# Kernel optimization log

Hardware: AMD Instinct MI355X
Metric: run time of the kernel (lower is better)

## Reference

```python
import jax, jax.numpy as jnp
import numpy as np

EPS = 1e-5

def bn(x, gamma, beta, axes):
    # Training-mode batch norm: normalize over batch(+spatial) axes, channel-last layout.
    m = x.mean(axes, keepdims=True)
    v = x.var(axes, keepdims=True)
    return gamma * (x - m) * jax.lax.rsqrt(v + EPS) + beta

def spa_group(k, xyz, feat):
    # PCT-style grouping: k-NN in xyz space, concat(neighbor-center, center).
    # xyz: (B,N,3)  feat: (B,N,C)  ->  (B,N,k,2C)
    sq = jnp.sum(xyz * xyz, axis=-1)  # (B,N)
    d = sq[:, :, None] + sq[:, None, :] - 2.0 * jnp.einsum('bnd,bmd->bnm', xyz, xyz)
    _, idx = jax.lax.top_k(-d, k)  # (B,N,k) nearest-neighbor indices (includes self)
    grouped = jax.vmap(lambda f, i: f[i])(feat, idx)  # (B,N,k,C) irregular gather
    center = feat[:, :, None, :]
    return jnp.concatenate([grouped - center, jnp.broadcast_to(center, grouped.shape)], axis=-1)

def local_op(x, w1, g1, b1, w2, g2, b2):
    # x: (B,N,K,Ci) -> conv1x1/BN/ReLU x2 over the K window, then max-pool over K -> (B,N,Co)
    h = jnp.einsum('bnkc,oc->bnko', x, w1)
    h = jax.nn.relu(bn(h, g1, b1, (0, 1, 2)))
    h = jnp.einsum('bnkc,oc->bnko', h, w2)
    h = jax.nn.relu(bn(h, g2, b2, (0, 1, 2)))
    return h.max(axis=2)

def setup_inputs():
    key = jax.random.key(0)
    ks = jax.random.split(key, 7)
    B, N = 4, 2048
    d_i, d_h1, d_h2, d_h3, d_o = 3, 64, 256, 512, 1024
    def w(k_, o, i):
        return jax.random.normal(k_, (o, i), jnp.float32) * (1.0 / np.sqrt(i))
    return {
        'xyz': jax.random.normal(ks[0], (B, N, d_i), jnp.float32),
        'w_c1': w(ks[1], d_h1, d_i), 'g_c1': jnp.ones((d_h1,), jnp.float32), 'b_c1': jnp.zeros((d_h1,), jnp.float32),
        'w_c2': w(ks[2], d_h2, d_h1), 'g_c2': jnp.ones((d_h2,), jnp.float32), 'b_c2': jnp.zeros((d_h2,), jnp.float32),
        'w_l0a': w(ks[3], d_h3, d_h3), 'g_l0a': jnp.ones((d_h3,), jnp.float32), 'b_l0a': jnp.zeros((d_h3,), jnp.float32),
        'w_l0b': w(ks[4], d_h3, d_h3), 'g_l0b': jnp.ones((d_h3,), jnp.float32), 'b_l0b': jnp.zeros((d_h3,), jnp.float32),
        'w_l1a': w(ks[5], d_o, d_o), 'g_l1a': jnp.ones((d_o,), jnp.float32), 'b_l1a': jnp.zeros((d_o,), jnp.float32),
        'w_l1b': w(ks[6], d_o, d_o), 'g_l1b': jnp.ones((d_o,), jnp.float32), 'b_l1b': jnp.zeros((d_o,), jnp.float32),
        'k': 8,
    }

def reference(xyz, w_c1, g_c1, b_c1, w_c2, g_c2, b_c2,
              w_l0a, g_l0a, b_l0a, w_l0b, g_l0b, b_l0b,
              w_l1a, g_l1a, b_l1a, w_l1b, g_l1b, b_l1b, k):
    # Stem: conv1x1-BN-ReLU x2 in (B,N,C) layout (equivalent to torch (B,C,N) with BN over (0,2))
    h = jax.nn.relu(bn(jnp.einsum('bnc,oc->bno', xyz, w_c1), g_c1, b_c1, (0, 1)))
    h = jax.nn.relu(bn(jnp.einsum('bnc,oc->bno', h, w_c2), g_c2, b_c2, (0, 1)))
    g = spa_group(k, xyz, h)                                   # (B,N,k,512)
    h = local_op(g, w_l0a, g_l0a, b_l0a, w_l0b, g_l0b, b_l0b)  # (B,N,512)
    g = spa_group(k, xyz, h)                                   # (B,N,k,1024)
    h = local_op(g, w_l1a, g_l1a, b_l1a, w_l1b, g_l1b, b_l1b)  # (B,N,1024)
    return jnp.transpose(h, (0, 2, 1))  # (B, d_o, N) to match torch output layout
```

## Files before the change

### kernel.cpp

```cpp
#include <hip/hip_runtime.h>

typedef unsigned short u16;
typedef __attribute__((ext_vector_type(8))) short s16x8;
typedef __attribute__((ext_vector_type(8))) __bf16 bf16x8;
typedef __attribute__((ext_vector_type(8))) unsigned short u16x8;
typedef __attribute__((ext_vector_type(4))) float f32x4;

#define BN_EPS 1e-5f

__device__ u16   g_Z[(size_t)65536 * 1024];
__device__ float g_pooled[(size_t)8192 * 1024];
__device__ float g_h2pre[8192 * 256];
__device__ u16   g_h2b[8192 * 256];
__device__ u16   g_hl0b[8192 * 512];
__device__ float g_y1[8192 * 64];
__device__ u16   g_wm0a[512 * 512];
__device__ u16   g_w0b[512 * 512];
__device__ u16   g_wm1a[1024 * 1024];
__device__ u16   g_w1b[1024 * 1024];
__device__ int   g_nidx[65536];
__device__ float g_st[24 * 1024];

#define S(i) (g_st + (i) * 1024)

static __device__ __forceinline__ float bf2f(u16 u) {
  unsigned int x = ((unsigned int)u) << 16;
  return __builtin_bit_cast(float, x);
}
static __device__ __forceinline__ u16 f2bf(float f) {
  unsigned int x = __builtin_bit_cast(unsigned int, f);
  x += 0x7fffu + ((x >> 16) & 1u);
  return (u16)(x >> 16);
}
static __device__ __forceinline__ f32x4 mfma16x16(s16x8 a, s16x8 b, f32x4 c) {
  return __builtin_amdgcn_mfma_f32_16x16x32_bf16(
      __builtin_bit_cast(bf16x8, a), __builtin_bit_cast(bf16x8, b), c, 0, 0, 0);
}
static __device__ __forceinline__ void gl_lds16(const void* g, void* l) {
  __builtin_amdgcn_global_load_lds((const __attribute__((address_space(1))) void*)g,
                                   (__attribute__((address_space(3))) void*)l, 16, 0, 0);
}

__global__ void k_zero() {
  int i = blockIdx.x * 256 + threadIdx.x;
  if (i < 12 * 1024) g_st[i] = 0.f;
}

__global__ void k_lin1(const float* __restrict__ xyz, const float* __restrict__ w) {
  __shared__ float ls[64], lq[64];
  int t = threadIdx.x;
  if (t < 64) { ls[t] = 0.f; lq[t] = 0.f; }
  __syncthreads();
  int e = blockIdx.x * 256 + t;
  int row = e >> 6, ch = e & 63;
  float x0 = xyz[row * 3], x1 = xyz[row * 3 + 1], x2 = xyz[row * 3 + 2];
  float v = x0 * w[ch * 3] + x1 * w[ch * 3 + 1] + x2 * w[ch * 3 + 2];
  g_y1[e] = v;
  atomicAdd(&ls[ch], v);
  atomicAdd(&lq[ch], v * v);
  __syncthreads();
  if (t < 64) { atomicAdd(&S(0)[t], ls[t]); atomicAdd(&S(1)[t], lq[t]); }
}

__global__ void k_stats(const float* __restrict__ g, const float* __restrict__ b,
                        int si_s, int si_q, int si_sc, int si_bi, float invcnt) {
  int c = blockIdx.x * 64 + threadIdx.x;
  float m = S(si_s)[c] * invcnt;
  float v = S(si_q)[c] * invcnt - m * m;
  float sc = g[c] * rsqrtf(v + BN_EPS);
  S(si_sc)[c] = sc;
  S(si_bi)[c] = b[c] - m * sc;
}

__global__ void k_lin2(const float* __restrict__ w) {
  __shared__ float hrow[64];
  int t = threadIdx.x;
  float wr[64];
#pragma unroll
  for (int i = 0; i < 64; i++) wr[i] = w[t * 64 + i];
  const float* sc1 = S(12);
  const float* bi1 = S(13);
  float ps = 0.f, pq = 0.f;
  int r0 = blockIdx.x * 16;
  for (int r = 0; r < 16; r++) {
    if (t < 64) {
      float v = g_y1[(r0 + r) * 64 + t];
      v = v * sc1[t] + bi1[t];
      hrow[t] = v > 0.f ? v : 0.f;
    }
    __syncthreads();
    float acc = 0.f;
#pragma unroll
    for (int i = 0; i < 64; i++) acc += hrow[i] * wr[i];
    g_h2pre[(r0 + r) * 256 + t] = acc;
    ps += acc;
    pq += acc * acc;
    __syncthreads();
  }
  atomicAdd(&S(2)[t], ps);
  atomicAdd(&S(3)[t], pq);
}

__global__ void k_bnrelu_h2() {
  int i = blockIdx.x * 256 + threadIdx.x;
  if (i >= 8192 * 256) return;
  int c = i & 255;
  float v = g_h2pre[i] * S(14)[c] + S(15)[c];
  g_h2b[i] = f2bf(v > 0.f ? v : 0.f);
}

__global__ __launch_bounds__(256) void k_knn(const float* __restrict__ xyz) {
  int t = threadIdx.x, lane = t & 63, w = t >> 6;
  int qn = blockIdx.x * 4 + w;
  int b = qn >> 11;
  const float* xb = xyz + (size_t)b * 2048 * 3;
  int ql = qn & 2047;
  float qx = xb[ql * 3], qy = xb[ql * 3 + 1], qz = xb[ql * 3 + 2];
  float qsq = qx * qx + qy * qy + qz * qz;

  float bd[8];
  int bi[8];
#pragma unroll
  for (int i = 0; i < 8; i++) { bd[i] = 1e30f; bi[i] = 0x7fffffff; }

#pragma unroll 4
  for (int i = 0; i < 32; i++) {
    int j = lane + i * 64;
    float x = xb[j * 3], y = xb[j * 3 + 1], z = xb[j * 3 + 2];
    float sq = x * x + y * y + z * z;
    float d = qsq + sq - 2.0f * (qx * x + qy * y + qz * z);
    if (d < bd[7]) {
      bd[7] = d; bi[7] = j;
#pragma unroll
      for (int p = 7; p > 0; p--) {
        if (bd[p] < bd[p - 1]) {
          float td = bd[p]; bd[p] = bd[p - 1]; bd[p - 1] = td;
          int ti = bi[p]; bi[p] = bi[p - 1]; bi[p - 1] = ti;
        }
      }
    }
  }

  int keep = 0;
#pragma unroll
  for (int r = 0; r < 8; r++) {
    float md = bd[0];
    int mi = bi[0];
#pragma unroll
    for (int s = 1; s < 64; s <<= 1) {
      float od = __shfl_xor(md, s, 64);
      int oi = __shfl_xor(mi, s, 64);
      if (od < md || (od == md && oi < mi)) { md = od; mi = oi; }
    }
    bool own = (bd[0] == md) && (bi[0] == mi);
    if (own) {
#pragma unroll
      for (int p = 0; p < 7; p++) { bd[p] = bd[p + 1]; bi[p] = bi[p + 1]; }
      bd[7] = 1e30f; bi[7] = 0x7fffffff;
    }
    if (lane == r) keep = mi;
  }
  if (lane < 8) g_nidx[qn * 8 + lane] = b * 2048 + keep;
}

__global__ void k_prep_w(const float* __restrict__ src, int which, int K, int half, int n) {
  int i = blockIdx.x * 256 + threadIdx.x;
  if (i >= n) return;
  int col = i % K;
  float v = src[i];
  if (half && col >= half) v -= src[i - half];
  u16* dst = which == 0 ? g_wm0a : which == 1 ? g_w0b : which == 2 ? g_wm1a : g_w1b;
  dst[i] = f2bf(v);
}


#define GEMM_PRO()                                                     \
  int t = threadIdx.x, lane = t & 63, w = t >> 6;                      \
  int chunk = gridDim.x >> 3;                                          \
  int idx = ((int)blockIdx.x & 7) * chunk + ((int)blockIdx.x >> 3);    \
  int bx = idx & ((1 << lbx) - 1), by = idx >> lbx;                    \
  int wm = w >> 2, wn = w & 3;                                         \
  int l15 = lane & 15, lq = lane >> 4;                                 \
  int gcs = (((lane & 3) ^ ((lane >> 3) & 3))) * 8;                    \
  int rA0 = w * 16 + (lane >> 2), rA1 = rA0 + 128;                     \
  int ldsA0 = w * 512, ldsA1 = 4096 + w * 512;                         \
  int ksw = (lq ^ ((l15 >> 1) & 3)) * 8;                               \
  f32x4 acc[8][4];                                                     \
  _Pragma("unroll") for (int m = 0; m < 8; m++)                        \
  _Pragma("unroll") for (int n = 0; n < 4; n++)                        \
      acc[m][n] = f32x4{0.f, 0.f, 0.f, 0.f};

#define GEMM_LOOP(STG)                                                   \
  STG(0, 0) STG(1, 1) STG(2, 2)                                          \
  asm volatile("s_waitcnt vmcnt(8)" ::: "memory");                       \
  __builtin_amdgcn_s_barrier();                                          \
  asm volatile("" ::: "memory");                                         \
  for (int ks = 0; ks < nk; ks++) {                                      \
    int b = ks & 3;                                                      \
    int kst = (ks + 3 < nk) ? ks + 3 : nk - 1;                           \
    STG(kst, (ks + 3) & 3)                                               \
    s16x8 af[8], bf[4];                                                  \
    _Pragma("unroll") for (int m = 0; m < 8; m++)                        \
        af[m] = *(const s16x8*)&As[b][(wm * 128 + m * 16 + l15) * 32 + ksw]; \
    _Pragma("unroll") for (int n = 0; n < 4; n++)                        \
        bf[n] = *(const s16x8*)&Bs[b][(wn * 64 + n * 16 + l15) * 32 + ksw];  \
    __builtin_amdgcn_s_setprio(1);                                       \
    _Pragma("unroll") for (int m = 0; m < 8; m++)                        \
    _Pragma("unroll") for (int n = 0; n < 4; n++)                        \
        acc[m][n] = mfma16x16(af[m], bf[n], acc[m][n]);                  \
    __builtin_amdgcn_s_setprio(0);                                       \
    asm volatile("s_waitcnt vmcnt(8)" ::: "memory");                     \
    __builtin_amdgcn_s_barrier();                                        \
    asm volatile("" ::: "memory");                                       \
  }

#define GEMM_STATS(si_s, si_q)                                           \
  if (t < 256) { cs[t] = 0.f; cq[t] = 0.f; }                             \
  __syncthreads();                                                       \
  _Pragma("unroll") for (int n = 0; n < 4; n++) {                        \
    float ssum = 0.f, ssq = 0.f;                                         \
    _Pragma("unroll") for (int m = 0; m < 8; m++)                        \
    _Pragma("unroll") for (int j = 0; j < 4; j++) {                      \
      float v = acc[m][n][j];                                            \
      ssum += v;                                                         \
      ssq += v * v;                                                      \
    }                                                                    \
    int col = wn * 64 + n * 16 + l15;                                    \
    atomicAdd(&cs[col], ssum);                                           \
    atomicAdd(&cq[col], ssq);                                            \
  }                                                                      \
  __syncthreads();                                                       \
  if (t < 256) {                                                         \
    atomicAdd(&S(si_s)[bx * 256 + t], cs[t]);                            \
    atomicAdd(&S(si_q)[bx * 256 + t], cq[t]);                            \
  }

__global__ __launch_bounds__(512) void k_gg8(int layer, int C, int N, int si_s,
                                             int si_q, int lbx) {
  __shared__ u16 As[4][8192];
  __shared__ u16 Bs[4][8192];
  __shared__ float cs[256], cq[256];
  const u16* feat = layer == 0 ? g_h2b : g_hl0b;
  const u16* W = layer == 0 ? g_wm0a : g_wm1a;
  GEMM_PRO();
  int K = 2 * C, nk = K >> 5;
  int RA0 = by * 256 + rA0, RA1 = RA0 + 128;
  int nb0 = g_nidx[RA0], nb1 = g_nidx[RA1];
  int ct0 = RA0 >> 3, ct1 = RA1 >> 3;
  const u16* srB0 = W + (size_t)(bx * 256 + rA0) * K + gcs;
  const u16* srB1 = W + (size_t)(bx * 256 + rA1) * K + gcs;

#define STG_G(KT, BUF)                                                        \
  {                                                                           \
    int kg_ = (KT) * 32;                                                      \
    const u16 *sa0, *sa1;                                                     \
    if (kg_ < C) {                                                            \
      sa0 = feat + (size_t)nb0 * C + kg_ + gcs;                               \
      sa1 = feat + (size_t)nb1 * C + kg_ + gcs;                               \
    } else {                                                                  \
      sa0 = feat + (size_t)ct0 * C + (kg_ - C) + gcs;                         \
      sa1 = feat + (size_t)ct1 * C + (kg_ - C) + gcs;                         \
    }                                                                         \
    gl_lds16(sa0, &As[BUF][ldsA0]);                                           \
    gl_lds16(sa1, &As[BUF][ldsA1]);                                           \
    gl_lds16(srB0 + kg_, &Bs[BUF][ldsA0]);                                    \
    gl_lds16(srB1 + kg_, &Bs[BUF][ldsA1]);                                    \
  }

  GEMM_LOOP(STG_G)
#undef STG_G

#pragma unroll
  for (int m = 0; m < 8; m++) {
    int rbase = by * 256 + wm * 128 + m * 16 + lq * 4;
#pragma unroll
    for (int n = 0; n < 4; n++) {
      int col = bx * 256 + wn * 64 + n * 16 + l15;
#pragma unroll
      for (int j = 0; j < 4; j++)
        g_Z[(size_t)(rbase + j) * N + col] = f2bf(acc[m][n][j]);
    }
  }
  GEMM_STATS(si_s, si_q)
}

__global__ __launch_bounds__(512) void k_gp8(int layer, int K, int N, int si_s,
                                             int si_q, int lbx) {
  __shared__ u16 As[4][8192];
  __shared__ u16 Bs[4][8192];
  __shared__ float cs[256], cq[256];
  const u16* W = layer == 0 ? g_w0b : g_w1b;
  GEMM_PRO();
  int nk = K >> 5;
  const u16* srA0 = g_Z + (size_t)(by * 256 + rA0) * K + gcs;
  const u16* srA1 = g_Z + (size_t)(by * 256 + rA1) * K + gcs;
  const u16* srB0 = W + (size_t)(bx * 256 + rA0) * K + gcs;
  const u16* srB1 = W + (size_t)(bx * 256 + rA1) * K + gcs;

#define STG_P(KT, BUF)                                                        \
  {                                                                           \
    int kg_ = (KT) * 32;                                                      \
    gl_lds16(srA0 + kg_, &As[BUF][ldsA0]);                                    \
    gl_lds16(srA1 + kg_, &As[BUF][ldsA1]);                                    \
    gl_lds16(srB0 + kg_, &Bs[BUF][ldsA0]);                                    \
    gl_lds16(srB1 + kg_, &Bs[BUF][ldsA1]);                                    \
  }

  GEMM_LOOP(STG_P)
#undef STG_P

#pragma unroll
  for (int m = 0; m < 8; m++) {
    int prow = by * 32 + wm * 16 + m * 2 + (lq >> 1);
#pragma unroll
    for (int n = 0; n < 4; n++) {
      float v4 = fmaxf(fmaxf(acc[m][n][0], acc[m][n][1]), fmaxf(acc[m][n][2], acc[m][n][3]));
      float v8 = fmaxf(v4, __shfl_xor(v4, 16, 64));
      if ((lane & 16) == 0) {
        int col = bx * 256 + wn * 64 + n * 16 + l15;
        g_pooled[(size_t)prow * N + col] = v8;
      }
    }
  }
  GEMM_STATS(si_s, si_q)
}

__global__ void k_bnrelu_z(int si_sc, int si_bi, int cmask, size_t n8) {
  size_t i = (size_t)blockIdx.x * 256 + threadIdx.x;
  size_t stride = (size_t)gridDim.x * 256;
  const float* sc = S(si_sc);
  const float* bi = S(si_bi);
  for (; i < n8; i += stride) {
    u16x8 v = *(const u16x8*)(g_Z + i * 8);
    int c0 = (int)((i * 8) & (size_t)cmask);
    u16x8 o;
#pragma unroll
    for (int j = 0; j < 8; j++) {
      float f = bf2f(v[j]) * sc[c0 + j] + bi[c0 + j];
      o[j] = f2bf(f > 0.f ? f : 0.f);
    }
    *(u16x8*)(g_Z + i * 8) = o;
  }
}

__global__ void k_bnrelu_pool() {
  int i = blockIdx.x * 256 + threadIdx.x;
  if (i >= 8192 * 512) return;
  int c = i & 511;
  float v = g_pooled[i] * S(18)[c] + S(19)[c];
  g_hl0b[i] = f2bf(v > 0.f ? v : 0.f);
}

__global__ void k_final_t(float* __restrict__ out) {
  __shared__ float tile[64][65];
  int b = blockIdx.z;
  int nb = blockIdx.y;
  int cb = blockIdx.x;
  int t = threadIdx.x;
  int cl = t & 63;
  int c = cb * 64 + cl;
  float sc = S(22)[c], bi = S(23)[c];
  for (int nl = t >> 6; nl < 64; nl += 4) {
    float v = g_pooled[(size_t)(b * 2048 + nb * 64 + nl) * 1024 + c] * sc + bi;
    tile[nl][cl] = v > 0.f ? v : 0.f;
  }
  __syncthreads();
  int nl2 = t & 63;
  for (int ci = t >> 6; ci < 64; ci += 4) {
    out[((size_t)b * 1024 + cb * 64 + ci) * 2048 + nb * 64 + nl2] = tile[nl2][ci];
  }
}

extern "C" void kernel_launch(void* const* d_in, const int* in_sizes, int n_in,
                              void* d_out, int out_size, void* d_ws, size_t ws_size,
                              hipStream_t stream) {
  const float* xyz  = (const float*)d_in[0];
  const float* w_c1 = (const float*)d_in[1];
  const float* g_c1 = (const float*)d_in[2];
  const float* b_c1 = (const float*)d_in[3];
  const float* w_c2 = (const float*)d_in[4];
  const float* g_c2 = (const float*)d_in[5];
  const float* b_c2 = (const float*)d_in[6];
  const float* w_l0a = (const float*)d_in[7];
  const float* g_l0a = (const float*)d_in[8];
  const float* b_l0a = (const float*)d_in[9];
  const float* w_l0b = (const float*)d_in[10];
  const float* g_l0b = (const float*)d_in[11];
  const float* b_l0b = (const float*)d_in[12];
  const float* w_l1a = (const float*)d_in[13];
  const float* g_l1a = (const float*)d_in[14];
  const float* b_l1a = (const float*)d_in[15];
  const float* w_l1b = (const float*)d_in[16];
  const float* g_l1b = (const float*)d_in[17];
  const float* b_l1b = (const float*)d_in[18];
  float* out = (float*)d_out;

  k_zero<<<48, 256, 0, stream>>>();

  k_lin1<<<2048, 256, 0, stream>>>(xyz, w_c1);
  k_stats<<<1, 64, 0, stream>>>(g_c1, b_c1, 0, 1, 12, 13, 1.f / 8192.f);
  k_lin2<<<512, 256, 0, stream>>>(w_c2);
  k_stats<<<4, 64, 0, stream>>>(g_c2, b_c2, 2, 3, 14, 15, 1.f / 8192.f);
  k_bnrelu_h2<<<8192, 256, 0, stream>>>();

  k_knn<<<2048, 256, 0, stream>>>(xyz);

  k_prep_w<<<1024, 256, 0, stream>>>(w_l0a, 0, 512, 256, 262144);
  k_prep_w<<<1024, 256, 0, stream>>>(w_l0b, 1, 512, 0, 262144);
  k_prep_w<<<4096, 256, 0, stream>>>(w_l1a, 2, 1024, 512, 1048576);
  k_prep_w<<<4096, 256, 0, stream>>>(w_l1b, 3, 1024, 0, 1048576);

  k_gg8<<<512, 512, 0, stream>>>(0, 256, 512, 4, 5, 1);
  k_stats<<<8, 64, 0, stream>>>(g_l0a, b_l0a, 4, 5, 16, 17, 1.f / 65536.f);
  k_bnrelu_z<<<2048, 256, 0, stream>>>(16, 17, 511, (size_t)65536 * 512 / 8);
  k_gp8<<<512, 512, 0, stream>>>(0, 512, 512, 6, 7, 1);
  k_stats<<<8, 64, 0, stream>>>(g_l0b, b_l0b, 6, 7, 18, 19, 1.f / 65536.f);
  k_bnrelu_pool<<<16384, 256, 0, stream>>>();

  k_gg8<<<1024, 512, 0, stream>>>(1, 512, 1024, 8, 9, 2);
  k_stats<<<16, 64, 0, stream>>>(g_l1a, b_l1a, 8, 9, 20, 21, 1.f / 65536.f);
  k_bnrelu_z<<<2048, 256, 0, stream>>>(20, 21, 1023, (size_t)65536 * 1024 / 8);
  k_gp8<<<1024, 512, 0, stream>>>(1, 1024, 1024, 10, 11, 2);
  k_stats<<<16, 64, 0, stream>>>(g_l1b, b_l1b, 10, 11, 22, 23, 1.f / 65536.f);
  k_final_t<<<dim3(16, 32, 4), 256, 0, stream>>>(out);
}
```

Measured before the change: 897.6 us.

## Apply first local conv per point before gather, then combine gathered outputs

The first conv of each local_op is linear, so W·[f_nb - f_c, f_c] is split into W1·f_nb + (W2-W1)·f_c. Both products are now computed once per point (8192 rows) by a dense GEMM into a new buffer, replacing the per-neighbor GEMM over 65536 gathered rows with doubled K. A new combine kernel gathers the neighbor and center halves, adds them, writes Z in bf16 and accumulates the BN statistics. This cuts the matmul FLOPs for the first conv by roughly 8x, at the cost of an extra bf16 rounding of the intermediate sums and a memory-bound gather pass.

```diff
diff --git a/kernel.cpp b/kernel.cpp
--- a/kernel.cpp
+++ b/kernel.cpp
@@ -9,14 +9,15 @@
 #define BN_EPS 1e-5f
 
 __device__ u16   g_Z[(size_t)65536 * 1024];
+__device__ u16   g_F[(size_t)8192 * 2048];
 __device__ float g_pooled[(size_t)8192 * 1024];
 __device__ float g_h2pre[8192 * 256];
 __device__ u16   g_h2b[8192 * 256];
 __device__ u16   g_hl0b[8192 * 512];
 __device__ float g_y1[8192 * 64];
-__device__ u16   g_wm0a[512 * 512];
+__device__ u16   g_wm0a[1024 * 256];
 __device__ u16   g_w0b[512 * 512];
-__device__ u16   g_wm1a[1024 * 1024];
+__device__ u16   g_wm1a[2048 * 512];
 __device__ u16   g_w1b[1024 * 1024];
 __device__ int   g_nidx[65536];
 __device__ float g_st[24 * 1024];
@@ -163,13 +164,22 @@
   if (lane < 8) g_nidx[qn * 8 + lane] = b * 2048 + keep;
 }
 
-__global__ void k_prep_w(const float* __restrict__ src, int which, int K, int half, int n) {
+__global__ void k_prep_w(const float* __restrict__ src, int which, int n) {
   int i = blockIdx.x * 256 + threadIdx.x;
   if (i >= n) return;
-  int col = i % K;
-  float v = src[i];
-  if (half && col >= half) v -= src[i - half];
-  u16* dst = which == 0 ? g_wm0a : which == 1 ? g_w0b : which == 2 ? g_wm1a : g_w1b;
+  u16* dst = which == 1 ? g_w0b : g_w1b;
+  dst[i] = f2bf(src[i]);
+}
+
+__global__ void k_prep_wst(const float* __restrict__ src, int which, int lc, int N, int n) {
+  int i = blockIdx.x * 256 + threadIdx.x;
+  if (i >= n) return;
+  int C = 1 << lc;
+  int r = i >> lc, c = i & (C - 1);
+  float v;
+  if (r < N) v = src[r * 2 * C + c];
+  else { int o = r - N; v = src[o * 2 * C + C + c] - src[o * 2 * C + c]; }
+  u16* dst = which == 0 ? g_wm0a : g_wm1a;
   dst[i] = f2bf(v);
 }
 
@@ -235,40 +245,29 @@
     atomicAdd(&S(si_q)[bx * 256 + t], cq[t]);                            \
   }
 
-__global__ __launch_bounds__(512) void k_gg8(int layer, int C, int N, int si_s,
-                                             int si_q, int lbx) {
+__global__ __launch_bounds__(512) void k_fgemm(int layer, int C, int N2, int lbx) {
   __shared__ u16 As[4][8192];
   __shared__ u16 Bs[4][8192];
-  __shared__ float cs[256], cq[256];
   const u16* feat = layer == 0 ? g_h2b : g_hl0b;
   const u16* W = layer == 0 ? g_wm0a : g_wm1a;
   GEMM_PRO();
-  int K = 2 * C, nk = K >> 5;
-  int RA0 = by * 256 + rA0, RA1 = RA0 + 128;
-  int nb0 = g_nidx[RA0], nb1 = g_nidx[RA1];
-  int ct0 = RA0 >> 3, ct1 = RA1 >> 3;
-  const u16* srB0 = W + (size_t)(bx * 256 + rA0) * K + gcs;
-  const u16* srB1 = W + (size_t)(bx * 256 + rA1) * K + gcs;
-
-#define STG_G(KT, BUF)                                                        \
+  int nk = C >> 5;
+  const u16* srA0 = feat + (size_t)(by * 256 + rA0) * C + gcs;
+  const u16* srA1 = feat + (size_t)(by * 256 + rA1) * C + gcs;
+  const u16* srB0 = W + (size_t)(bx * 256 + rA0) * C + gcs;
+  const u16* srB1 = W + (size_t)(bx * 256 + rA1) * C + gcs;
+
+#define STG_F(KT, BUF)                                                        \
   {                                                                           \
     int kg_ = (KT) * 32;                                                      \
-    const u16 *sa0, *sa1;                                                     \
-    if (kg_ < C) {                                                            \
-      sa0 = feat + (size_t)nb0 * C + kg_ + gcs;                               \
-      sa1 = feat + (size_t)nb1 * C + kg_ + gcs;                               \
-    } else {                                                                  \
-      sa0 = feat + (size_t)ct0 * C + (kg_ - C) + gcs;                         \
-      sa1 = feat + (size_t)ct1 * C + (kg_ - C) + gcs;                         \
-    }                                                                         \
-    gl_lds16(sa0, &As[BUF][ldsA0]);                                           \
-    gl_lds16(sa1, &As[BUF][ldsA1]);                                           \
+    gl_lds16(srA0 + kg_, &As[BUF][ldsA0]);                                    \
+    gl_lds16(srA1 + kg_, &As[BUF][ldsA1]);                                    \
     gl_lds16(srB0 + kg_, &Bs[BUF][ldsA0]);                                    \
     gl_lds16(srB1 + kg_, &Bs[BUF][ldsA1]);                                    \
   }
 
-  GEMM_LOOP(STG_G)
-#undef STG_G
+  GEMM_LOOP(STG_F)
+#undef STG_F
 
 #pragma unroll
   for (int m = 0; m < 8; m++) {
@@ -278,10 +277,54 @@
       int col = bx * 256 + wn * 64 + n * 16 + l15;
 #pragma unroll
       for (int j = 0; j < 4; j++)
-        g_Z[(size_t)(rbase + j) * N + col] = f2bf(acc[m][n][j]);
-    }
-  }
-  GEMM_STATS(si_s, si_q)
+        g_F[(size_t)(rbase + j) * N2 + col] = f2bf(acc[m][n][j]);
+    }
+  }
+}
+
+__global__ __launch_bounds__(512) void k_combine(int N, int lgc, int si_s, int si_q) {
+  __shared__ float Ls[1024], Lq[1024];
+  int t = threadIdx.x;
+  int chs8 = 1 << lgc;
+  int c8 = t & (chs8 - 1);
+  int g = t >> lgc;
+  int G = 512 >> lgc;
+  int rpg = 256 / G;
+  int row0 = blockIdx.x * 256 + g * rpg;
+  int ch0 = c8 * 8;
+  int N2 = 2 * N;
+  float ss[8], sq[8];
+#pragma unroll
+  for (int j = 0; j < 8; j++) { ss[j] = 0.f; sq[j] = 0.f; }
+
+  for (int r = row0; r < row0 + rpg; r++) {
+    int nb = g_nidx[r];
+    int ct = r >> 3;
+    u16x8 a = *(const u16x8*)(g_F + (size_t)nb * N2 + ch0);
+    u16x8 b = *(const u16x8*)(g_F + (size_t)ct * N2 + N + ch0);
+    u16x8 o;
+#pragma unroll
+    for (int j = 0; j < 8; j++) {
+      float z = bf2f(a[j]) + bf2f(b[j]);
+      o[j] = f2bf(z);
+      ss[j] += z;
+      sq[j] += z * z;
+    }
+    *(u16x8*)(g_Z + (size_t)r * N + ch0) = o;
+  }
+
+  for (int c = t; c < N; c += 512) { Ls[c] = 0.f; Lq[c] = 0.f; }
+  __syncthreads();
+#pragma unroll
+  for (int j = 0; j < 8; j++) {
+    atomicAdd(&Ls[ch0 + j], ss[j]);
+    atomicAdd(&Lq[ch0 + j], sq[j]);
+  }
+  __syncthreads();
+  for (int c = t; c < N; c += 512) {
+    atomicAdd(&S(si_s)[c], Ls[c]);
+    atomicAdd(&S(si_q)[c], Lq[c]);
+  }
 }
 
 __global__ __launch_bounds__(512) void k_gp8(int layer, int K, int N, int si_s,
@@ -405,19 +448,21 @@
 
   k_knn<<<2048, 256, 0, stream>>>(xyz);
 
-  k_prep_w<<<1024, 256, 0, stream>>>(w_l0a, 0, 512, 256, 262144);
-  k_prep_w<<<1024, 256, 0, stream>>>(w_l0b, 1, 512, 0, 262144);
-  k_prep_w<<<4096, 256, 0, stream>>>(w_l1a, 2, 1024, 512, 1048576);
-  k_prep_w<<<4096, 256, 0, stream>>>(w_l1b, 3, 1024, 0, 1048576);
-
-  k_gg8<<<512, 512, 0, stream>>>(0, 256, 512, 4, 5, 1);
+  k_prep_wst<<<1024, 256, 0, stream>>>(w_l0a, 0, 8, 512, 262144);
+  k_prep_w<<<1024, 256, 0, stream>>>(w_l0b, 1, 262144);
+  k_prep_wst<<<4096, 256, 0, stream>>>(w_l1a, 2, 9, 1024, 1048576);
+  k_prep_w<<<4096, 256, 0, stream>>>(w_l1b, 3, 1048576);
+
+  k_fgemm<<<128, 512, 0, stream>>>(0, 256, 1024, 2);
+  k_combine<<<256, 512, 0, stream>>>(512, 6, 4, 5);
   k_stats<<<8, 64, 0, stream>>>(g_l0a, b_l0a, 4, 5, 16, 17, 1.f / 65536.f);
   k_bnrelu_z<<<2048, 256, 0, stream>>>(16, 17, 511, (size_t)65536 * 512 / 8);
   k_gp8<<<512, 512, 0, stream>>>(0, 512, 512, 6, 7, 1);
   k_stats<<<8, 64, 0, stream>>>(g_l0b, b_l0b, 6, 7, 18, 19, 1.f / 65536.f);
   k_bnrelu_pool<<<16384, 256, 0, stream>>>();
 
-  k_gg8<<<1024, 512, 0, stream>>>(1, 512, 1024, 8, 9, 2);
+  k_fgemm<<<256, 512, 0, stream>>>(1, 512, 2048, 3);
+  k_combine<<<256, 512, 0, stream>>>(1024, 7, 8, 9);
   k_stats<<<16, 64, 0, stream>>>(g_l1a, b_l1a, 8, 9, 20, 21, 1.f / 65536.f);
   k_bnrelu_z<<<2048, 256, 0, stream>>>(20, 21, 1023, (size_t)65536 * 1024 / 8);
   k_gp8<<<1024, 512, 0, stream>>>(1, 1024, 1024, 10, 11, 2);
```

After: 773.4 us. 13.8% less time.
